# Kernel optimization log

Hardware: AMD Instinct MI355X
Metric: run time of the kernel (lower is better)

The kernel has to match this reference:

```python
import jax, jax.numpy as jnp
import numpy as np

V = 50257   # vocab_size
E = 512     # word_vec_size
H = 512     # hidden_size
L = 2       # num_layers
SOS = 1     # sos_id


def setup_inputs() -> dict:
    key = jax.random.key(0)
    ks = jax.random.split(key, 14)
    B, T, S = 32, 32, 128
    return {
        'tgt_seqs': jax.random.randint(ks[0], (B, T), 0, V),
        'decoder_hidden': jax.random.normal(ks[1], (L, B, H), jnp.float32) * 0.1,
        'encoder_outputs': jax.random.normal(ks[2], (S, B, H), jnp.float32),
        'attention_mask': jnp.zeros((B, S), dtype=bool),  # True = masked position
        'emb_W': jax.random.normal(ks[3], (V, E), jnp.float32) * 0.02,
        'gru_Wih': jax.random.normal(ks[4], (L, 3 * H, E), jnp.float32) * 0.02,
        'gru_Whh': jax.random.normal(ks[5], (L, 3 * H, H), jnp.float32) * 0.02,
        'gru_bih': jnp.zeros((L, 3 * H), jnp.float32),
        'gru_bhh': jnp.zeros((L, 3 * H), jnp.float32),
        'Wa': jax.random.normal(ks[6], (H, H), jnp.float32) * 0.02,
        'ba': jnp.zeros((H,), jnp.float32),
        'Wc': jax.random.normal(ks[7], (H, 2 * H), jnp.float32) * 0.02,
        'bc': jnp.zeros((H,), jnp.float32),
        'Ws': jax.random.normal(ks[8], (V, H), jnp.float32) * 0.02,
        'bs': jnp.zeros((V,), jnp.float32),
    }


def reference(tgt_seqs, decoder_hidden, encoder_outputs, attention_mask,
              emb_W, gru_Wih, gru_Whh, gru_bih, gru_bhh,
              Wa, ba, Wc, bc, Ws, bs):
    B, T = tgt_seqs.shape
    Hh = decoder_hidden.shape[-1]
    enc = jnp.transpose(encoder_outputs, (1, 0, 2))            # (B, S, H)
    enc_proj = jnp.einsum('bsh,gh->bsg', enc, Wa) + ba         # W_a(enc), precomputed
    # teacher-forced inputs: sos then shifted targets, time-major (T, B)
    tokens = jnp.concatenate(
        [jnp.full((B, 1), SOS, tgt_seqs.dtype), tgt_seqs[:, :-1]], axis=1).T

    def step(h, tok):
        x = emb_W[tok]                                          # (B, E)
        hs = []
        for l in range(L):                                      # small fixed layer loop
            gx = x @ gru_Wih[l].T + gru_bih[l]
            gh = h[l] @ gru_Whh[l].T + gru_bhh[l]
            r = jax.nn.sigmoid(gx[:, :Hh] + gh[:, :Hh])
            z = jax.nn.sigmoid(gx[:, Hh:2 * Hh] + gh[:, Hh:2 * Hh])
            n = jnp.tanh(gx[:, 2 * Hh:] + r * gh[:, 2 * Hh:])
            x = (1.0 - z) * n + z * h[l]
            hs.append(x)
        h_new = jnp.stack(hs)                                   # (L, B, H)
        # Luong general attention
        scores = jnp.einsum('bh,bsh->bs', x, enc_proj)          # (B, S)
        scores = jnp.where(attention_mask, -1e9, scores)
        attn = jax.nn.softmax(scores, axis=-1)
        ctx = jnp.einsum('bs,bsh->bh', attn, enc)               # (B, H)
        concat = jnp.tanh(jnp.concatenate([ctx, x], axis=-1) @ Wc.T + bc)
        return h_new, concat

    h_final, concats = jax.lax.scan(step, decoder_hidden, tokens)  # concats: (T, B, H)
    decoder_outputs = jnp.einsum('tbh,vh->tbv', concats, Ws) + bs  # (T, B, V)
    return decoder_outputs, h_final
```

## Files before the change

kernel.cpp:

```cpp
#include <hip/hip_runtime.h>
#include <hip/hip_bf16.h>
#include <stdint.h>
#include <stddef.h>

#define B_ 32
#define T_ 32
#define S_ 128
#define H_ 512
#define V_ 50257
#define VPAD 50304
#define TH3 1536

typedef __attribute__((ext_vector_type(8))) short short8x;
typedef __attribute__((ext_vector_type(4))) float f32x4;

__device__ __forceinline__ float sigf(float x) { return 1.f / (1.f + __expf(-x)); }
__device__ __forceinline__ float tanhfast(float x) {
  float e = __expf(2.f * x);
  return 1.f - 2.f / (e + 1.f);
}
__device__ __forceinline__ unsigned short f2bf(float x) {
  unsigned int u = __float_as_uint(x);
  return (unsigned short)((u + 0x7fffu + ((u >> 16) & 1u)) >> 16);
}
__device__ __forceinline__ float dot4(float4 a, float4 b) {
  return a.x * b.x + a.y * b.y + a.z * b.z + a.w * b.w;
}

__device__ __forceinline__ void async16(const unsigned short* g, short* l) {
  __builtin_amdgcn_global_load_lds(
      (const __attribute__((address_space(1))) unsigned int*)g,
      (__attribute__((address_space(3))) unsigned int*)l, 16, 0, 0);
}

__device__ __forceinline__ void gridbar(int* bar, int ep) {
  __syncthreads();
  if (blockIdx.x == 0) {
    if (threadIdx.x > 0) {
      const int* f = bar + threadIdx.x * 32;
      while (__hip_atomic_load(f, __ATOMIC_RELAXED, __HIP_MEMORY_SCOPE_AGENT) < ep)
        __builtin_amdgcn_s_sleep(1);
    }
    __syncthreads();
    if (threadIdx.x == 0) {
      __hip_atomic_store(bar + 8192, ep, __ATOMIC_RELEASE, __HIP_MEMORY_SCOPE_AGENT);
      __builtin_amdgcn_fence(__ATOMIC_ACQUIRE, "agent");
    }
    __syncthreads();
  } else {
    if (threadIdx.x == 0) {
      __hip_atomic_store(bar + (int)blockIdx.x * 32, ep, __ATOMIC_RELEASE,
                         __HIP_MEMORY_SCOPE_AGENT);
      const int* g = bar + 8192;
      while (__hip_atomic_load(g, __ATOMIC_RELAXED, __HIP_MEMORY_SCOPE_AGENT) < ep)
        __builtin_amdgcn_s_sleep(1);
      __builtin_amdgcn_fence(__ATOMIC_ACQUIRE, "agent");
    }
    __syncthreads();
  }
}

__global__ __launch_bounds__(256) void cvt_kernel(const float* __restrict__ Ws,
                                                  unsigned short* __restrict__ outb) {
  size_t i = ((size_t)blockIdx.x * 256 + threadIdx.x) * 4;
  if (i >= (size_t)VPAD * 512) return;
  float4 f;
  if (i < (size_t)V_ * 512) f = *(const float4*)(Ws + i);
  else f = make_float4(0.f, 0.f, 0.f, 0.f);
  ushort4 u;
  u.x = f2bf(f.x); u.y = f2bf(f.y); u.z = f2bf(f.z); u.w = f2bf(f.w);
  *(ushort4*)(outb + i) = u;
}

template <int MODE>
__global__ __launch_bounds__(256) void gemm_f32(const float* __restrict__ Asrc,
                                                const float* __restrict__ Bw,
                                                const float* __restrict__ bias,
                                                float* __restrict__ Cout,
                                                const int* __restrict__ tgt, int N) {
  __shared__ __align__(16) float As[16][68];
  __shared__ __align__(16) float Bs[16][68];
  const int tid = threadIdx.x;
  const int tx = tid & 15, ty = tid >> 4;
  const int m0 = blockIdx.y * 64, n0 = blockIdx.x * 64;
  const int srow = tid >> 2, skq = (tid & 3) * 4;
  const float* arow;
  {
    int m = m0 + srow;
    if (MODE == 0) {
      int t = m >> 5, b = m & 31;
      int tok = (t == 0) ? 1 : tgt[b * 32 + t - 1];
      arow = Asrc + (size_t)tok * 512;
    } else {
      int b = m >> 7, s = m & 127;
      arow = Asrc + ((size_t)s * 32 + b) * 512;
    }
  }
  const float* brow = Bw + (size_t)(n0 + srow) * 512;
  float acc[4][4] = {};
  for (int k0 = 0; k0 < 512; k0 += 16) {
    float4 av = *(const float4*)(arow + k0 + skq);
    float4 bv = *(const float4*)(brow + k0 + skq);
    __syncthreads();
    As[skq + 0][srow] = av.x; As[skq + 1][srow] = av.y;
    As[skq + 2][srow] = av.z; As[skq + 3][srow] = av.w;
    Bs[skq + 0][srow] = bv.x; Bs[skq + 1][srow] = bv.y;
    Bs[skq + 2][srow] = bv.z; Bs[skq + 3][srow] = bv.w;
    __syncthreads();
#pragma unroll
    for (int kk = 0; kk < 16; ++kk) {
      float4 a4 = *(const float4*)&As[kk][ty * 4];
      float4 b4 = *(const float4*)&Bs[kk][tx * 4];
      acc[0][0] += a4.x * b4.x; acc[0][1] += a4.x * b4.y; acc[0][2] += a4.x * b4.z; acc[0][3] += a4.x * b4.w;
      acc[1][0] += a4.y * b4.x; acc[1][1] += a4.y * b4.y; acc[1][2] += a4.y * b4.z; acc[1][3] += a4.y * b4.w;
      acc[2][0] += a4.z * b4.x; acc[2][1] += a4.z * b4.y; acc[2][2] += a4.z * b4.z; acc[2][3] += a4.z * b4.w;
      acc[3][0] += a4.w * b4.x; acc[3][1] += a4.w * b4.y; acc[3][2] += a4.w * b4.z; acc[3][3] += a4.w * b4.w;
    }
  }
  float4 b4 = *(const float4*)(bias + n0 + tx * 4);
#pragma unroll
  for (int i = 0; i < 4; ++i) {
    float4 o;
    o.x = acc[i][0] + b4.x; o.y = acc[i][1] + b4.y;
    o.z = acc[i][2] + b4.z; o.w = acc[i][3] + b4.w;
    *(float4*)(Cout + (size_t)(m0 + ty * 4 + i) * N + n0 + tx * 4) = o;
  }
}

__global__ __launch_bounds__(256) void seq_kernel(
    const float* __restrict__ dh, const float* __restrict__ enc,
    const unsigned char* __restrict__ mask,
    const float* __restrict__ Whh, const float* __restrict__ Wih,
    const float* __restrict__ bih, const float* __restrict__ bhh,
    const float* __restrict__ Wc, const float* __restrict__ bc,
    const float* __restrict__ gx0v, const float* __restrict__ encp,
    int* __restrict__ bar, float* __restrict__ x0buf, float* __restrict__ x1buf,
    float* __restrict__ attnbuf, float* __restrict__ ctxbuf,
    unsigned short* __restrict__ cbf, float* __restrict__ out_hf) {
  const int tid = threadIdx.x, bid = blockIdx.x;
  __shared__ __align__(16) float sm[3456];
  __shared__ __align__(16) float wlds[12288];
  const int lane = tid & 63, wv = tid >> 6;
  const int bb = lane & 31, rh = lane >> 5;

  if (bid < 64) {
    const int iset0 = bid * 8;
    for (int idx = tid; idx < 24 * 128; idx += 256) {
      const int rloc = idx >> 7, kq = (idx & 127) << 2;
      const int g = rloc >> 3, ii = rloc & 7;
      *(float4*)&wlds[rloc * 512 + kq] =
          *(const float4*)(Whh + (size_t)(g * 512 + iset0 + ii) * 512 + kq);
    }
  } else if (bid < 192) {
    const int iset0 = (bid - 64) * 4;
    for (int idx = tid; idx < 12 * 128; idx += 256) {
      const int rloc = idx >> 7, kq = (idx & 127) << 2;
      const int g = rloc >> 2, ii = rloc & 3;
      const size_t off = (size_t)(1536 + g * 512 + iset0 + ii) * 512 + kq;
      *(float4*)&wlds[rloc * 512 + kq] = *(const float4*)(Wih + off);
      *(float4*)&wlds[(12 + rloc) * 512 + kq] = *(const float4*)(Whh + off);
    }
  } else {
    const int gg0 = (bid < 224) ? (bid - 192) * 8 : 256 + (bid - 224) * 8;
    for (int idx = tid; idx < 8 * 256; idx += 256) {
      const int r = idx >> 8, kq = (idx & 255) << 2;
      *(float4*)&wlds[r * 1024 + kq] =
          *(const float4*)(Wc + (size_t)(gg0 + r) * 1024 + kq);
    }
  }
  __syncthreads();

  for (int p = -1; p <= 34; ++p) {
    if (bid < 64) {
      if (p <= 30) {
        const int iset0 = bid * 8;
        const float* xsrc = (p == -1) ? dh : (x0buf + (p & 1) * 16384);
        float acc[12];
#pragma unroll
        for (int r = 0; r < 12; ++r) acc[r] = 0.f;
        const float* xb = xsrc + bb * 512 + wv * 128;
        for (int c = 0; c < 4; ++c) {
          float4 xv[8];
#pragma unroll
          for (int u = 0; u < 8; ++u) xv[u] = *(const float4*)(xb + c * 32 + u * 4);
#pragma unroll
          for (int rr = 0; rr < 12; ++rr) {
            const int rloc = rh * 12 + rr;
            const float* wrow = wlds + (size_t)rloc * 512 + wv * 128 + c * 32;
#pragma unroll
            for (int u = 0; u < 8; ++u)
              acc[rr] += dot4(*(const float4*)(wrow + u * 4), xv[u]);
          }
        }
        __syncthreads();
#pragma unroll
        for (int rr = 0; rr < 12; ++rr)
          sm[wv * 768 + (rh * 12 + rr) * 32 + bb] = acc[rr];
        __syncthreads();
        {
          const int b2 = tid & 31, i2 = tid >> 5;
          const int ig = iset0 + i2;
          float s0 = bhh[ig], s1 = bhh[512 + ig], s2 = bhh[1024 + ig];
#pragma unroll
          for (int w = 0; w < 4; ++w) {
            s0 += sm[w * 768 + (i2) * 32 + b2];
            s1 += sm[w * 768 + (8 + i2) * 32 + b2];
            s2 += sm[w * 768 + (16 + i2) * 32 + b2];
          }
          const float* gx = gx0v + ((size_t)(p + 1) * 32 + b2) * 1536;
          const float hv = xsrc[b2 * 512 + ig];
          const float r = sigf(gx[ig] + s0);
          const float z = sigf(gx[512 + ig] + s1);
          const float n = tanhfast(gx[1024 + ig] + r * s2);
          const float xn = (1.f - z) * n + z * hv;
          x0buf[((p + 1) & 1) * 16384 + b2 * 512 + ig] = xn;
          if (p == 30) out_hf[b2 * 512 + ig] = xn;
        }
      }
    } else if (bid < 192) {
      if (p >= 0 && p <= 31) {
        const int iset0 = (bid - 64) * 4;
        const float* xs0 = x0buf + (p & 1) * 16384;
        const float* xs1 = (p == 0) ? (dh + 16384) : (x1buf + ((p - 1) & 3) * 16384);
        float acc[12];
#pragma unroll
        for (int r = 0; r < 12; ++r) acc[r] = 0.f;
        {
          const float* xb = xs0 + bb * 512 + wv * 128;
          for (int c = 0; c < 4; ++c) {
            float4 xv[8];
#pragma unroll
            for (int u = 0; u < 8; ++u) xv[u] = *(const float4*)(xb + c * 32 + u * 4);
#pragma unroll
            for (int rr = 0; rr < 6; ++rr) {
              const int rloc = rh * 6 + rr;
              const float* wrow = wlds + (size_t)rloc * 512 + wv * 128 + c * 32;
#pragma unroll
              for (int u = 0; u < 8; ++u)
                acc[rr] += dot4(*(const float4*)(wrow + u * 4), xv[u]);
            }
          }
        }
        {
          const float* xb = xs1 + bb * 512 + wv * 128;
          for (int c = 0; c < 4; ++c) {
            float4 xv[8];
#pragma unroll
            for (int u = 0; u < 8; ++u) xv[u] = *(const float4*)(xb + c * 32 + u * 4);
#pragma unroll
            for (int rr = 0; rr < 6; ++rr) {
              const int rloc = rh * 6 + rr;
              const float* wrow = wlds + (size_t)(12 + rloc) * 512 + wv * 128 + c * 32;
#pragma unroll
              for (int u = 0; u < 8; ++u)
                acc[6 + rr] += dot4(*(const float4*)(wrow + u * 4), xv[u]);
            }
          }
        }
        __syncthreads();
#pragma unroll
        for (int rr = 0; rr < 6; ++rr) {
          sm[wv * 768 + (rh * 6 + rr) * 32 + bb] = acc[rr];
          sm[wv * 768 + (12 + rh * 6 + rr) * 32 + bb] = acc[6 + rr];
        }
        __syncthreads();
        if (tid < 128) {
          const int b2 = tid & 31, i2 = tid >> 5;
          const int ig = iset0 + i2;
          float gxs[3], ghs[3];
#pragma unroll
          for (int g = 0; g < 3; ++g) {
            float a = bih[1536 + g * 512 + ig];
            float h = bhh[1536 + g * 512 + ig];
#pragma unroll
            for (int w = 0; w < 4; ++w) {
              a += sm[w * 768 + (g * 4 + i2) * 32 + b2];
              h += sm[w * 768 + (12 + g * 4 + i2) * 32 + b2];
            }
            gxs[g] = a; ghs[g] = h;
          }
          const float hv = xs1[b2 * 512 + ig];
          const float r = sigf(gxs[0] + ghs[0]);
          const float z = sigf(gxs[1] + ghs[1]);
          const float n = tanhfast(gxs[2] + r * ghs[2]);
          const float xn = (1.f - z) * n + z * hv;
          x1buf[(p & 3) * 16384 + b2 * 512 + ig] = xn;
          if (p == 31) out_hf[16384 + b2 * 512 + ig] = xn;
        }
      }
    } else if (bid < 224) {
      const int b = bid - 192;
      if (p >= 1 && p <= 32) {
        const int t = p - 1;
        const float* x1 = x1buf + (t & 3) * 16384 + b * 512;
        const int s = tid >> 1, kh = tid & 1;
        const float* ep = encp + ((size_t)b * 128 + s) * 512 + kh * 256;
        const float* xx = x1 + kh * 256;
        float a = 0.f;
#pragma unroll 8
        for (int k = 0; k < 256; k += 4)
          a += dot4(*(const float4*)(ep + k), *(const float4*)(xx + k));
        sm[tid] = a;
        __syncthreads();
        if (tid < 128) {
          float sc = sm[2 * tid] + sm[2 * tid + 1];
          if (mask[b * 128 + tid]) sc = -1e9f;
          sm[256 + tid] = sc;
        }
        __syncthreads();
        if (tid < 64) {
          float m1 = fmaxf(sm[256 + tid], sm[256 + tid + 64]);
#pragma unroll
          for (int off = 32; off; off >>= 1) m1 = fmaxf(m1, __shfl_xor(m1, off));
          float e0 = __expf(sm[256 + tid] - m1), e1 = __expf(sm[256 + tid + 64] - m1);
          float ssum = e0 + e1;
#pragma unroll
          for (int off = 32; off; off >>= 1) ssum += __shfl_xor(ssum, off);
          float inv = 1.f / ssum;
          sm[384 + tid] = e0 * inv;
          sm[384 + tid + 64] = e1 * inv;
        }
        __syncthreads();
        if (tid < 128) attnbuf[(t & 1) * 4096 + b * 128 + tid] = sm[384 + tid];
      }
      if (p >= 3) {
        const int t = p - 3;
        const int gg = (bid - 192) * 8 + (tid >> 5);
        const int b2 = tid & 31;
        const float* ctx = ctxbuf + (t & 1) * 16384 + b2 * 512;
        const float* x1c = x1buf + (t & 3) * 16384 + b2 * 512;
        const float* wr = wlds + (size_t)(tid >> 5) * 1024;
        float a = bc[gg];
#pragma unroll 4
        for (int k = 0; k < 512; k += 4) a += dot4(*(const float4*)(wr + k), *(const float4*)(ctx + k));
#pragma unroll 4
        for (int k = 0; k < 512; k += 4) a += dot4(*(const float4*)(wr + 512 + k), *(const float4*)(x1c + k));
        cbf[((size_t)t * 32 + b2) * 512 + gg] = f2bf(tanhfast(a));
      }
    } else {
      const int b = bid - 224;
      if (p >= 2 && p <= 33) {
        const int t = p - 2;
        if (tid < 128) sm[tid] = attnbuf[(t & 1) * 4096 + b * 128 + tid];
        __syncthreads();
        if (tid < 128) {
          const int h4 = tid * 4;
          float4 c = make_float4(0.f, 0.f, 0.f, 0.f);
#pragma unroll 8
          for (int s = 0; s < 128; ++s) {
            const float a = sm[s];
            const float4 e = *(const float4*)(enc + ((size_t)s * 32 + b) * 512 + h4);
            c.x += a * e.x; c.y += a * e.y; c.z += a * e.z; c.w += a * e.w;
          }
          *(float4*)(ctxbuf + (t & 1) * 16384 + b * 512 + h4) = c;
        }
        __syncthreads();
      }
      if (p >= 3) {
        const int t = p - 3;
        const int gg = 256 + (bid - 224) * 8 + (tid >> 5);
        const int b2 = tid & 31;
        const float* ctx = ctxbuf + (t & 1) * 16384 + b2 * 512;
        const float* x1c = x1buf + (t & 3) * 16384 + b2 * 512;
        const float* wr = wlds + (size_t)(tid >> 5) * 1024;
        float a = bc[gg];
#pragma unroll 4
        for (int k = 0; k < 512; k += 4) a += dot4(*(const float4*)(wr + k), *(const float4*)(ctx + k));
#pragma unroll 4
        for (int k = 0; k < 512; k += 4) a += dot4(*(const float4*)(wr + 512 + k), *(const float4*)(x1c + k));
        cbf[((size_t)t * 32 + b2) * 512 + gg] = f2bf(tanhfast(a));
      }
    }
    if (p < 34) gridbar(bar, p + 2);
  }
}

__global__ __launch_bounds__(256) void proj_kernel(const unsigned short* __restrict__ A,
                                                   const unsigned short* __restrict__ Bw,
                                                   const float* __restrict__ bs,
                                                   float* __restrict__ C) {
  __shared__ short8x AsV[512];
  __shared__ short8x BsV[512];
  short* As = (short*)AsV;
  short* Bs = (short*)BsV;
  const int tid = threadIdx.x;
  const int lane = tid & 63, wv = tid >> 6;
  const int m0 = blockIdx.x * 128;
  const int n0 = blockIdx.y * 128;
  const int wm = (wv >> 1) * 64, wn = (wv & 1) * 64;
  f32x4 acc[4][4] = {};
  const int sr = lane >> 2, sb = (lane & 3) * 8;
  const unsigned short* gA1 = A + (size_t)(m0 + wv * 16 + sr) * 512 + sb;
  const unsigned short* gA2 = gA1 + (size_t)64 * 512;
  const unsigned short* gB1 = Bw + (size_t)(n0 + wv * 16 + sr) * 512 + sb;
  const unsigned short* gB2 = gB1 + (size_t)64 * 512;
  short* lA1 = As + (wv * 16) * 32;
  short* lA2 = As + (64 + wv * 16) * 32;
  short* lB1 = Bs + (wv * 16) * 32;
  short* lB2 = Bs + (64 + wv * 16) * 32;
  const int rA = wm + (lane & 15);
  const int rB = wn + (lane & 15);
  const int kb = (lane >> 4) * 8;
  for (int kt = 0; kt < 16; ++kt) {
    const int ko = kt * 32;
    __syncthreads();
    async16(gA1 + ko, lA1);
    async16(gA2 + ko, lA2);
    async16(gB1 + ko, lB1);
    async16(gB2 + ko, lB2);
    __syncthreads();
    short8x af[4], bf[4];
#pragma unroll
    for (int i = 0; i < 4; ++i) af[i] = *(const short8x*)(As + (rA + i * 16) * 32 + kb);
#pragma unroll
    for (int i = 0; i < 4; ++i) bf[i] = *(const short8x*)(Bs + (rB + i * 16) * 32 + kb);
#pragma unroll
    for (int mo = 0; mo < 4; ++mo)
#pragma unroll
      for (int no = 0; no < 4; ++no)
        acc[mo][no] = __builtin_amdgcn_mfma_f32_16x16x32_bf16(af[mo], bf[no], acc[mo][no], 0, 0, 0);
  }
#pragma unroll
  for (int no = 0; no < 4; ++no) {
    const int col = n0 + wn + no * 16 + (lane & 15);
    if (col < V_) {
      const float bsv = bs[col];
#pragma unroll
      for (int mo = 0; mo < 4; ++mo) {
        const int row = m0 + wm + mo * 16 + ((lane >> 4) << 2);
        f32x4 v = acc[mo][no];
        C[(size_t)(row + 0) * V_ + col] = v[0] + bsv;
        C[(size_t)(row + 1) * V_ + col] = v[1] + bsv;
        C[(size_t)(row + 2) * V_ + col] = v[2] + bsv;
        C[(size_t)(row + 3) * V_ + col] = v[3] + bsv;
      }
    }
  }
}

extern "C" void kernel_launch(void* const* d_in, const int* in_sizes, int n_in,
                              void* d_out, int out_size, void* d_ws, size_t ws_size,
                              hipStream_t stream) {
  (void)in_sizes; (void)n_in; (void)out_size; (void)ws_size;
  const int* tgt = (const int*)d_in[0];
  const float* dh = (const float*)d_in[1];
  const float* enc = (const float*)d_in[2];
  const unsigned char* mask = (const unsigned char*)d_in[3];
  const float* embW = (const float*)d_in[4];
  const float* Wih = (const float*)d_in[5];
  const float* Whh = (const float*)d_in[6];
  const float* bih = (const float*)d_in[7];
  const float* bhh = (const float*)d_in[8];
  const float* Wa = (const float*)d_in[9];
  const float* ba = (const float*)d_in[10];
  const float* Wc = (const float*)d_in[11];
  const float* bc = (const float*)d_in[12];
  const float* Ws = (const float*)d_in[13];
  const float* bs = (const float*)d_in[14];
  float* out = (float*)d_out;

  char* w = (char*)d_ws;
  int* bar = (int*)w;
  float* x0buf = (float*)(w + 40960);
  float* x1buf = x0buf + 32768;
  float* attnbuf = x1buf + 65536;
  float* ctxbuf = attnbuf + 8192;
  float* gx0v = ctxbuf + 32768;
  float* encp = gx0v + 1572864;
  unsigned short* cbf = (unsigned short*)(encp + 2097152);
  unsigned short* wsb = cbf + 524288;

  hipMemsetAsync(bar, 0, 40960, stream);
  cvt_kernel<<<25152, 256, 0, stream>>>(Ws, wsb);
  gemm_f32<0><<<dim3(24, 16), 256, 0, stream>>>(embW, Wih, bih, gx0v, tgt, 1536);
  gemm_f32<1><<<dim3(8, 64), 256, 0, stream>>>(enc, Wa, ba, encp, nullptr, 512);
  seq_kernel<<<256, 256, 0, stream>>>(dh, enc, mask, Whh, Wih, bih, bhh, Wc, bc,
                                      gx0v, encp, bar, x0buf, x1buf, attnbuf, ctxbuf,
                                      cbf, out + (size_t)1024 * V_);
  proj_kernel<<<dim3(8, 393), 256, 0, stream>>>(cbf, wsb, bs, out);
}
```

Before: 2.161 ms.

## Replace centralized grid barrier with all-to-all flag polling and write-through stores

The grid barrier no longer routes through block 0. Each block now publishes its own epoch flag, and 64 threads per block poll all 256 flags, which removes one round-trip of latency per step. Inter-block buffers are written with write-through stores (sc0 sc1), and their release/acquire fences are replaced by a vmcnt wait. The double and quad ring buffers become full per-timestep buffers, which avoids reuse hazards under the weaker barrier. The cost is much more polling traffic per barrier and reliance on relaxed system-scope atomics plus cache-bypassing stores for correctness instead of proper fences.

```diff
diff --git a/kernel.cpp b/kernel.cpp
--- a/kernel.cpp
+++ b/kernel.cpp
@@ -33,31 +33,34 @@
       (__attribute__((address_space(3))) unsigned int*)l, 16, 0, 0);
 }
 
+__device__ __forceinline__ void store_wt(float* p, float v) {
+  asm volatile("global_store_dword %0, %1, off sc0 sc1" :: "v"(p), "v"(v) : "memory");
+}
+__device__ __forceinline__ void store_wt4(float* p, f32x4 v) {
+  asm volatile("global_store_dwordx4 %0, %1, off sc0 sc1" :: "v"(p), "v"(v) : "memory");
+}
+
 __device__ __forceinline__ void gridbar(int* bar, int ep) {
+  asm volatile("s_waitcnt vmcnt(0)" ::: "memory");
   __syncthreads();
-  if (blockIdx.x == 0) {
-    if (threadIdx.x > 0) {
-      const int* f = bar + threadIdx.x * 32;
-      while (__hip_atomic_load(f, __ATOMIC_RELAXED, __HIP_MEMORY_SCOPE_AGENT) < ep)
-        __builtin_amdgcn_s_sleep(1);
-    }
-    __syncthreads();
-    if (threadIdx.x == 0) {
-      __hip_atomic_store(bar + 8192, ep, __ATOMIC_RELEASE, __HIP_MEMORY_SCOPE_AGENT);
-      __builtin_amdgcn_fence(__ATOMIC_ACQUIRE, "agent");
-    }
-    __syncthreads();
-  } else {
-    if (threadIdx.x == 0) {
-      __hip_atomic_store(bar + (int)blockIdx.x * 32, ep, __ATOMIC_RELEASE,
-                         __HIP_MEMORY_SCOPE_AGENT);
-      const int* g = bar + 8192;
-      while (__hip_atomic_load(g, __ATOMIC_RELAXED, __HIP_MEMORY_SCOPE_AGENT) < ep)
-        __builtin_amdgcn_s_sleep(1);
-      __builtin_amdgcn_fence(__ATOMIC_ACQUIRE, "agent");
-    }
-    __syncthreads();
-  }
+  const int tid = threadIdx.x;
+  if (tid == 0)
+    __hip_atomic_store(bar + (int)blockIdx.x * 32, ep, __ATOMIC_RELAXED,
+                       __HIP_MEMORY_SCOPE_SYSTEM);
+  if (tid < 64) {
+    int got = 0;
+    while (got != 15) {
+#pragma unroll
+      for (int j = 0; j < 4; ++j)
+        if (!((got >> j) & 1)) {
+          int v = __hip_atomic_load(bar + (tid * 4 + j) * 32, __ATOMIC_RELAXED,
+                                    __HIP_MEMORY_SCOPE_SYSTEM);
+          if (v >= ep) got |= (1 << j);
+        }
+      if (got != 15) __builtin_amdgcn_s_sleep(2);
+    }
+  }
+  __syncthreads();
 }
 
 __global__ __launch_bounds__(256) void cvt_kernel(const float* __restrict__ Ws,
@@ -174,7 +177,7 @@
     if (bid < 64) {
       if (p <= 30) {
         const int iset0 = bid * 8;
-        const float* xsrc = (p == -1) ? dh : (x0buf + (p & 1) * 16384);
+        const float* xsrc = (p == -1) ? dh : (x0buf + (size_t)p * 16384);
         float acc[12];
 #pragma unroll
         for (int r = 0; r < 12; ++r) acc[r] = 0.f;
@@ -213,15 +216,15 @@
           const float z = sigf(gx[512 + ig] + s1);
           const float n = tanhfast(gx[1024 + ig] + r * s2);
           const float xn = (1.f - z) * n + z * hv;
-          x0buf[((p + 1) & 1) * 16384 + b2 * 512 + ig] = xn;
+          store_wt(x0buf + (size_t)(p + 1) * 16384 + b2 * 512 + ig, xn);
           if (p == 30) out_hf[b2 * 512 + ig] = xn;
         }
       }
     } else if (bid < 192) {
       if (p >= 0 && p <= 31) {
         const int iset0 = (bid - 64) * 4;
-        const float* xs0 = x0buf + (p & 1) * 16384;
-        const float* xs1 = (p == 0) ? (dh + 16384) : (x1buf + ((p - 1) & 3) * 16384);
+        const float* xs0 = x0buf + (size_t)p * 16384;
+        const float* xs1 = (p == 0) ? (dh + 16384) : (x1buf + (size_t)(p - 1) * 16384);
         float acc[12];
 #pragma unroll
         for (int r = 0; r < 12; ++r) acc[r] = 0.f;
@@ -284,7 +287,7 @@
           const float z = sigf(gxs[1] + ghs[1]);
           const float n = tanhfast(gxs[2] + r * ghs[2]);
           const float xn = (1.f - z) * n + z * hv;
-          x1buf[(p & 3) * 16384 + b2 * 512 + ig] = xn;
+          store_wt(x1buf + (size_t)p * 16384 + b2 * 512 + ig, xn);
           if (p == 31) out_hf[16384 + b2 * 512 + ig] = xn;
         }
       }
@@ -292,7 +295,7 @@
       const int b = bid - 192;
       if (p >= 1 && p <= 32) {
         const int t = p - 1;
-        const float* x1 = x1buf + (t & 3) * 16384 + b * 512;
+        const float* x1 = x1buf + (size_t)t * 16384 + b * 512;
         const int s = tid >> 1, kh = tid & 1;
         const float* ep = encp + ((size_t)b * 128 + s) * 512 + kh * 256;
         const float* xx = x1 + kh * 256;
@@ -321,14 +324,14 @@
           sm[384 + tid + 64] = e1 * inv;
         }
         __syncthreads();
-        if (tid < 128) attnbuf[(t & 1) * 4096 + b * 128 + tid] = sm[384 + tid];
+        if (tid < 128) store_wt(attnbuf + (size_t)t * 4096 + b * 128 + tid, sm[384 + tid]);
       }
       if (p >= 3) {
         const int t = p - 3;
         const int gg = (bid - 192) * 8 + (tid >> 5);
         const int b2 = tid & 31;
-        const float* ctx = ctxbuf + (t & 1) * 16384 + b2 * 512;
-        const float* x1c = x1buf + (t & 3) * 16384 + b2 * 512;
+        const float* ctx = ctxbuf + (size_t)t * 16384 + b2 * 512;
+        const float* x1c = x1buf + (size_t)t * 16384 + b2 * 512;
         const float* wr = wlds + (size_t)(tid >> 5) * 1024;
         float a = bc[gg];
 #pragma unroll 4
@@ -341,7 +344,7 @@
       const int b = bid - 224;
       if (p >= 2 && p <= 33) {
         const int t = p - 2;
-        if (tid < 128) sm[tid] = attnbuf[(t & 1) * 4096 + b * 128 + tid];
+        if (tid < 128) sm[tid] = attnbuf[(size_t)t * 4096 + b * 128 + tid];
         __syncthreads();
         if (tid < 128) {
           const int h4 = tid * 4;
@@ -352,7 +355,8 @@
             const float4 e = *(const float4*)(enc + ((size_t)s * 32 + b) * 512 + h4);
             c.x += a * e.x; c.y += a * e.y; c.z += a * e.z; c.w += a * e.w;
           }
-          *(float4*)(ctxbuf + (t & 1) * 16384 + b * 512 + h4) = c;
+          f32x4 cc = {c.x, c.y, c.z, c.w};
+          store_wt4(ctxbuf + (size_t)t * 16384 + b * 512 + h4, cc);
         }
         __syncthreads();
       }
@@ -360,8 +364,8 @@
         const int t = p - 3;
         const int gg = 256 + (bid - 224) * 8 + (tid >> 5);
         const int b2 = tid & 31;
-        const float* ctx = ctxbuf + (t & 1) * 16384 + b2 * 512;
-        const float* x1c = x1buf + (t & 3) * 16384 + b2 * 512;
+        const float* ctx = ctxbuf + (size_t)t * 16384 + b2 * 512;
+        const float* x1c = x1buf + (size_t)t * 16384 + b2 * 512;
         const float* wr = wlds + (size_t)(tid >> 5) * 1024;
         float a = bc[gg];
 #pragma unroll 4
@@ -462,10 +466,10 @@
   char* w = (char*)d_ws;
   int* bar = (int*)w;
   float* x0buf = (float*)(w + 40960);
-  float* x1buf = x0buf + 32768;
-  float* attnbuf = x1buf + 65536;
-  float* ctxbuf = attnbuf + 8192;
-  float* gx0v = ctxbuf + 32768;
+  float* x1buf = x0buf + 524288;
+  float* attnbuf = x1buf + 524288;
+  float* ctxbuf = attnbuf + 131072;
+  float* gx0v = ctxbuf + 524288;
   float* encp = gx0v + 1572864;
   unsigned short* cbf = (unsigned short*)(encp + 2097152);
   unsigned short* wsb = cbf + 524288;
```

Result: faster. 1.933 ms (-10.6%).
